# Performance work log

Measured on AMD Instinct MI355X. Metric: run time of the kernel, lower is better.

Reference implementation:

```python
import jax, jax.numpy as jnp
import numpy as np

D = 1024
H = 16
HD = D // H
FF = 4096
B = 4
S = 1024
EPS = 1e-5


def layer_norm(x, g, b):
    mu = jnp.mean(x, axis=-1, keepdims=True)
    var = jnp.mean(jnp.square(x - mu), axis=-1, keepdims=True)
    return (x - mu) * jax.lax.rsqrt(var + EPS) * g + b


def setup_inputs() -> dict:
    key = jax.random.key(0)
    ks = jax.random.split(key, 16)
    s = 0.02
    return {
        "src": jax.random.normal(ks[0], (B, S, D), jnp.float32),
        "attn_bias": jax.random.normal(ks[1], (H, S, S), jnp.float32),
        "Wqkv": jax.random.normal(ks[2], (3 * D, D), jnp.float32) * s,
        "bqkv": jnp.zeros((3 * D,), jnp.float32),
        "Wo": jax.random.normal(ks[3], (D, D), jnp.float32) * s,
        "bo": jnp.zeros((D,), jnp.float32),
        "g1": jnp.ones((D,), jnp.float32),
        "b1n": jnp.zeros((D,), jnp.float32),
        "g2": jnp.ones((D,), jnp.float32),
        "b2n": jnp.zeros((D,), jnp.float32),
        "W1": jax.random.normal(ks[4], (FF, D), jnp.float32) * s,
        "b1": jnp.zeros((FF,), jnp.float32),
        "W2": jax.random.normal(ks[5], (D, FF), jnp.float32) * s,
        "b2": jnp.zeros((D,), jnp.float32),
    }


def reference(src, attn_bias, Wqkv, bqkv, Wo, bo, g1, b1n, g2, b2n, W1, b1, W2, b2):
    bsz, seq, _ = src.shape
    qkv = src @ Wqkv.T + bqkv                      # [B,S,3D]
    q, k, v = jnp.split(qkv, 3, axis=-1)
    q = q.reshape(bsz, seq, H, HD)
    k = k.reshape(bsz, seq, H, HD)
    v = v.reshape(bsz, seq, H, HD)
    scores = jnp.einsum('bthd,bshd->bhts', q, k) / np.sqrt(HD).astype(np.float32)
    scores = scores + attn_bias[None]              # 3D bias broadcast over batch
    w = jax.nn.softmax(scores, axis=-1)
    ctx = jnp.einsum('bhts,bshd->bthd', w, v).reshape(bsz, seq, D)
    attn_out = ctx @ Wo.T + bo
    x = layer_norm(src + attn_out, g1, b1n)
    ff = (jax.nn.gelu(x @ W1.T + b1, approximate=False)) @ W2.T + b2
    return layer_norm(x + ff, g2, b2n)
```

## Files before the change

### kernel.cpp

```cpp
#include <hip/hip_runtime.h>
#include <cstdint>

typedef unsigned short u16;
typedef __bf16 bf16x8 __attribute__((ext_vector_type(8)));
typedef float f32x4 __attribute__((ext_vector_type(4)));
typedef unsigned short u16x8 __attribute__((ext_vector_type(8)));
typedef unsigned short u16x4 __attribute__((ext_vector_type(4)));

__device__ __forceinline__ u16 f2b(float f) {
  union { float f; unsigned u; } x; x.f = f;
  unsigned r = (x.u + 0x7FFFu + ((x.u >> 16) & 1u)) >> 16;
  return (u16)r;
}
__device__ __forceinline__ float b2f(u16 v) {
  union { unsigned u; float f; } x; x.u = (unsigned)v << 16; return x.f;
}

__device__ __forceinline__ void gload_lds16(const void* g, void* l) {
  __builtin_amdgcn_global_load_lds(
      (__attribute__((address_space(1))) void*)(uintptr_t)g,
      (__attribute__((address_space(3))) void*)(uintptr_t)l, 16, 0, 0);
}

struct CastArgs {
  const float* in[5];
  u16* out[5];
  int cum[6];
};
__global__ void cast_multi(CastArgs a) {
  const int i = blockIdx.x * 256 + threadIdx.x;
  int r = 0;
#pragma unroll
  for (int k = 1; k < 5; ++k) r += (i >= a.cum[k]);
  const int local = i - a.cum[r];
  const float4 v = *(const float4*)(a.in[r] + (size_t)local * 4);
  u16x4 o = {f2b(v.x), f2b(v.y), f2b(v.z), f2b(v.w)};
  *(u16x4*)(a.out[r] + (size_t)local * 4) = o;
}

template<bool GELU_ACT, bool WRITE_VT>
__global__ void gemm_nt(const u16* __restrict__ A, const u16* __restrict__ Bw,
                        const float* __restrict__ bias, u16* __restrict__ Cb,
                        u16* __restrict__ Vt, int M, int N, int K) {
  __shared__ u16 As[2][128 * 32];
  __shared__ u16 Bs[2][128 * 32];
  const int tid = threadIdx.x;
  const int lane = tid & 63, wid = tid >> 6;
  const int bm = blockIdx.y * 128, bn = blockIdx.x * 128;
  const int wm = wid >> 1, wn = wid & 1;
  const int r = lane & 15, g = lane >> 4;
  const int s4 = (r >> 1) & 3;

  auto stage = [&](int buf, int k0) {
#pragma unroll
    for (int i = 0; i < 2; ++i) {
      const int c = tid + i * 256;
      const int row = c >> 2, ch = c & 3;
      const int gs = ch ^ ((row >> 1) & 3);
      gload_lds16(A + (size_t)(bm + row) * K + k0 + gs * 8, &As[buf][c * 8]);
      gload_lds16(Bw + (size_t)(bn + row) * K + k0 + gs * 8, &Bs[buf][c * 8]);
    }
  };

  f32x4 acc[4][4] = {};
  stage(0, 0);
  __syncthreads();
  const int nk = K >> 5;
  int cur = 0;
  for (int kt = 0; kt < nk; ++kt) {
    if (kt + 1 < nk) stage(cur ^ 1, (kt + 1) * 32);
    bf16x8 af[4], bfr[4];
#pragma unroll
    for (int m = 0; m < 4; ++m)
      af[m] = *(const bf16x8*)&As[cur][(wm * 64 + m * 16 + r) * 32 + (g ^ s4) * 8];
#pragma unroll
    for (int n = 0; n < 4; ++n)
      bfr[n] = *(const bf16x8*)&Bs[cur][(wn * 64 + n * 16 + r) * 32 + (g ^ s4) * 8];
#pragma unroll
    for (int m = 0; m < 4; ++m)
#pragma unroll
      for (int n = 0; n < 4; ++n)
        acc[m][n] = __builtin_amdgcn_mfma_f32_16x16x32_bf16(af[m], bfr[n], acc[m][n], 0, 0, 0);
    __syncthreads();
    cur ^= 1;
  }
#pragma unroll
  for (int m = 0; m < 4; ++m) {
    const int row0 = bm + wm * 64 + m * 16 + g * 4;
#pragma unroll
    for (int n = 0; n < 4; ++n) {
      const int col = bn + wn * 64 + n * 16 + r;
      const float bv = bias[col];
      if (WRITE_VT && col >= 2048) {
        const int hv = col - 2048;
        const int bb = row0 >> 10, s0 = row0 & 1023;
        u16x4 ov;
#pragma unroll
        for (int j = 0; j < 4; ++j) ov[j] = f2b(acc[m][n][j] + bv);
        *(u16x4*)(Vt + (((size_t)(bb * 16 + (hv >> 6))) * 64 + (hv & 63)) * 1024 + s0) = ov;
      } else {
#pragma unroll
        for (int j = 0; j < 4; ++j) {
          float v = acc[m][n][j] + bv;
          if (GELU_ACT) v = 0.5f * v * (1.f + erff(v * 0.70710678118654752f));
          Cb[(size_t)(row0 + j) * N + col] = f2b(v);
        }
      }
    }
  }
}

__global__ void gemm_nt_splitk(const u16* __restrict__ A, const u16* __restrict__ Bw,
                               float* __restrict__ parts, int M, int N, int K, int Kc) {
  __shared__ u16 As[2][128 * 32];
  __shared__ u16 Bs[2][128 * 32];
  const int tid = threadIdx.x;
  const int lane = tid & 63, wid = tid >> 6;
  const int bm = blockIdx.y * 128, bn = blockIdx.x * 128;
  const int kbase = blockIdx.z * Kc;
  const int wm = wid >> 1, wn = wid & 1;
  const int r = lane & 15, g = lane >> 4;
  const int s4 = (r >> 1) & 3;

  auto stage = [&](int buf, int k0) {
#pragma unroll
    for (int i = 0; i < 2; ++i) {
      const int c = tid + i * 256;
      const int row = c >> 2, ch = c & 3;
      const int gs = ch ^ ((row >> 1) & 3);
      gload_lds16(A + (size_t)(bm + row) * K + k0 + gs * 8, &As[buf][c * 8]);
      gload_lds16(Bw + (size_t)(bn + row) * K + k0 + gs * 8, &Bs[buf][c * 8]);
    }
  };

  f32x4 acc[4][4] = {};
  stage(0, kbase);
  __syncthreads();
  const int nk = Kc >> 5;
  int cur = 0;
  for (int kt = 0; kt < nk; ++kt) {
    if (kt + 1 < nk) stage(cur ^ 1, kbase + (kt + 1) * 32);
    bf16x8 af[4], bfr[4];
#pragma unroll
    for (int m = 0; m < 4; ++m)
      af[m] = *(const bf16x8*)&As[cur][(wm * 64 + m * 16 + r) * 32 + (g ^ s4) * 8];
#pragma unroll
    for (int n = 0; n < 4; ++n)
      bfr[n] = *(const bf16x8*)&Bs[cur][(wn * 64 + n * 16 + r) * 32 + (g ^ s4) * 8];
#pragma unroll
    for (int m = 0; m < 4; ++m)
#pragma unroll
      for (int n = 0; n < 4; ++n)
        acc[m][n] = __builtin_amdgcn_mfma_f32_16x16x32_bf16(af[m], bfr[n], acc[m][n], 0, 0, 0);
    __syncthreads();
    cur ^= 1;
  }
  float* Cp = parts + (size_t)blockIdx.z * M * N;
#pragma unroll
  for (int m = 0; m < 4; ++m) {
    const int row0 = bm + wm * 64 + m * 16 + g * 4;
#pragma unroll
    for (int n = 0; n < 4; ++n) {
      const int col = bn + wn * 64 + n * 16 + r;
#pragma unroll
      for (int j = 0; j < 4; ++j)
        Cp[(size_t)(row0 + j) * N + col] = acc[m][n][j];
    }
  }
}

__global__ __launch_bounds__(256) void attn_kernel(
    const u16* __restrict__ qkv, const u16* __restrict__ Vt,
    const float* __restrict__ bias, u16* __restrict__ ctx) {
  const int fid = blockIdx.x;
  const int xcd = fid & 7, slot = fid >> 3;
  const int G = xcd * 64 + (slot >> 2);
  const int b = slot & 3;
  const int h = G >> 5;
  const int q0 = (G & 31) * 32;
  const int tid = threadIdx.x;
  const int lane = tid & 63, wid = tid >> 6;
  const int r = lane & 15, g = lane >> 4;
  const int bh = b * 16 + h;

  __shared__ __align__(16) u16 PB[2][16 * 1024];

  const size_t qb0 = (size_t)(b * 1024 + q0 + r) * 3072 + h * 64;
  const size_t qb1 = (size_t)(b * 1024 + q0 + 16 + r) * 3072 + h * 64;
  const bf16x8 aq00 = *(const bf16x8*)(qkv + qb0 + g * 8);
  const bf16x8 aq01 = *(const bf16x8*)(qkv + qb0 + 32 + g * 8);
  const bf16x8 aq10 = *(const bf16x8*)(qkv + qb1 + g * 8);
  const bf16x8 aq11 = *(const bf16x8*)(qkv + qb1 + 32 + g * 8);

  const int n0 = wid * 256;

  const u16* kptr = qkv + (size_t)(b * 1024 + n0 + r) * 3072 + 1024 + h * 64;
  const size_t kstep = (size_t)16 * 3072;
  bf16x8 k0a = *(const bf16x8*)(kptr + g * 8);
  bf16x8 k1a = *(const bf16x8*)(kptr + 32 + g * 8);
#pragma unroll
  for (int nt = 0; nt < 16; ++nt) {
    bf16x8 k0b, k1b;
    if (nt + 1 < 16) {
      const u16* kn = kptr + (size_t)(nt + 1) * kstep;
      k0b = *(const bf16x8*)(kn + g * 8);
      k1b = *(const bf16x8*)(kn + 32 + g * 8);
    }
    f32x4 a0 = {0.f, 0.f, 0.f, 0.f}, a1 = {0.f, 0.f, 0.f, 0.f};
    a0 = __builtin_amdgcn_mfma_f32_16x16x32_bf16(k0a, aq00, a0, 0, 0, 0);
    a1 = __builtin_amdgcn_mfma_f32_16x16x32_bf16(k0a, aq10, a1, 0, 0, 0);
    a0 = __builtin_amdgcn_mfma_f32_16x16x32_bf16(k1a, aq01, a0, 0, 0, 0);
    a1 = __builtin_amdgcn_mfma_f32_16x16x32_bf16(k1a, aq11, a1, 0, 0, 0);
    const int col = n0 + nt * 16 + g * 4;
    const int idx = r * 1024 + (col ^ ((r & 15) << 3));
    u16x4 o0 = {f2b(a0[0] * 0.125f), f2b(a0[1] * 0.125f),
                f2b(a0[2] * 0.125f), f2b(a0[3] * 0.125f)};
    u16x4 o1 = {f2b(a1[0] * 0.125f), f2b(a1[1] * 0.125f),
                f2b(a1[2] * 0.125f), f2b(a1[3] * 0.125f)};
    *(u16x4*)&PB[0][idx] = o0;
    *(u16x4*)&PB[1][idx] = o1;
    k0a = k0b;
    k1a = k1b;
  }
  __syncthreads();

#pragma unroll
  for (int tr = 0; tr < 8; ++tr) {
    const int t = tr & 1, rr = tr >> 1;
    const int row = wid * 4 + rr;
    const int swz = (row & 15) << 3;
    u16* prow = &PB[t][row * 1024];
    const float* brow = bias + ((size_t)h * 1024 + q0 + t * 16 + row) * 1024;
    const int c0 = lane * 16;
    float bb[16];
    *(float4*)&bb[0]  = *(const float4*)(brow + c0);
    *(float4*)&bb[4]  = *(const float4*)(brow + c0 + 4);
    *(float4*)&bb[8]  = *(const float4*)(brow + c0 + 8);
    *(float4*)&bb[12] = *(const float4*)(brow + c0 + 12);
    const u16x8 v0 = *(const u16x8*)&prow[c0 ^ swz];
    const u16x8 v1 = *(const u16x8*)&prow[(c0 + 8) ^ swz];
    float f[16];
#pragma unroll
    for (int k = 0; k < 8; ++k) {
      f[k]     = b2f(v0[k]) + bb[k];
      f[8 + k] = b2f(v1[k]) + bb[8 + k];
    }
    float m = f[0];
#pragma unroll
    for (int k = 1; k < 16; ++k) m = fmaxf(m, f[k]);
    m = fmaxf(m, __shfl_xor(m, 1));  m = fmaxf(m, __shfl_xor(m, 2));
    m = fmaxf(m, __shfl_xor(m, 4));  m = fmaxf(m, __shfl_xor(m, 8));
    m = fmaxf(m, __shfl_xor(m, 16)); m = fmaxf(m, __shfl_xor(m, 32));
    float s = 0.f;
#pragma unroll
    for (int k = 0; k < 16; ++k) { f[k] = __expf(f[k] - m); s += f[k]; }
    s += __shfl_xor(s, 1);  s += __shfl_xor(s, 2);
    s += __shfl_xor(s, 4);  s += __shfl_xor(s, 8);
    s += __shfl_xor(s, 16); s += __shfl_xor(s, 32);
    const float inv = 1.f / s;
    u16x8 o0, o1;
#pragma unroll
    for (int k = 0; k < 8; ++k) {
      o0[k] = f2b(f[k] * inv);
      o1[k] = f2b(f[8 + k] * inv);
    }
    *(u16x8*)&prow[c0 ^ swz] = o0;
    *(u16x8*)&prow[(c0 + 8) ^ swz] = o1;
  }
  __syncthreads();

  f32x4 oa = {0.f, 0.f, 0.f, 0.f}, ob = {0.f, 0.f, 0.f, 0.f};
  const u16* vrow = Vt + ((size_t)bh * 64 + wid * 16 + r) * 1024;
  bf16x8 vba = *(const bf16x8*)(vrow + g * 8);
#pragma unroll
  for (int ks = 0; ks < 32; ++ks) {
    bf16x8 vbb;
    if (ks + 1 < 32) vbb = *(const bf16x8*)(vrow + (ks + 1) * 32 + g * 8);
    const int off = (ks * 32 + g * 8) ^ ((r & 15) << 3);
    const bf16x8 pa0 = *(const bf16x8*)&PB[0][r * 1024 + off];
    const bf16x8 pa1 = *(const bf16x8*)&PB[1][r * 1024 + off];
    oa = __builtin_amdgcn_mfma_f32_16x16x32_bf16(pa0, vba, oa, 0, 0, 0);
    ob = __builtin_amdgcn_mfma_f32_16x16x32_bf16(pa1, vba, ob, 0, 0, 0);
    vba = vbb;
  }
#pragma unroll
  for (int j = 0; j < 4; ++j) {
    ctx[(size_t)(b * 1024 + q0 + g * 4 + j) * 1024 + h * 64 + wid * 16 + r] = f2b(oa[j]);
    ctx[(size_t)(b * 1024 + q0 + 16 + g * 4 + j) * 1024 + h * 64 + wid * 16 + r] = f2b(ob[j]);
  }
}

template<int NP, bool RESID_BF16>
__global__ void ln_sum_kernel(const float* __restrict__ parts,
                              const void* __restrict__ resid,
                              const float* __restrict__ cbias,
                              const float* __restrict__ gw, const float* __restrict__ bw,
                              float* __restrict__ outf, u16* __restrict__ outb) {
  const int row = blockIdx.x, tid = threadIdx.x;
  const size_t off = (size_t)row * 1024 + tid * 4;
  float4 v;
  if (RESID_BF16) {
    const u16x4 rb = *(const u16x4*)((const u16*)resid + off);
    v.x = b2f(rb[0]); v.y = b2f(rb[1]); v.z = b2f(rb[2]); v.w = b2f(rb[3]);
  } else {
    v = *(const float4*)((const float*)resid + off);
  }
  const float4 cb = *(const float4*)(cbias + tid * 4);
  v.x += cb.x; v.y += cb.y; v.z += cb.z; v.w += cb.w;
#pragma unroll
  for (int p = 0; p < NP; ++p) {
    const float4 a = *(const float4*)(parts + (size_t)p * 4096 * 1024 + off);
    v.x += a.x; v.y += a.y; v.z += a.z; v.w += a.w;
  }
  float s = v.x + v.y + v.z + v.w;
  float q = v.x * v.x + v.y * v.y + v.z * v.z + v.w * v.w;
#pragma unroll
  for (int m = 32; m >= 1; m >>= 1) { s += __shfl_xor(s, m); q += __shfl_xor(q, m); }
  __shared__ float rs[4], rq[4];
  if ((tid & 63) == 0) { rs[tid >> 6] = s; rq[tid >> 6] = q; }
  __syncthreads();
  s = rs[0] + rs[1] + rs[2] + rs[3];
  q = rq[0] + rq[1] + rq[2] + rq[3];
  const float mu = s * (1.f / 1024.f);
  const float inv = rsqrtf(q * (1.f / 1024.f) - mu * mu + 1e-5f);
  const float4 g4 = *(const float4*)(gw + tid * 4);
  const float4 b4 = *(const float4*)(bw + tid * 4);
  float4 o;
  o.x = (v.x - mu) * inv * g4.x + b4.x;
  o.y = (v.y - mu) * inv * g4.y + b4.y;
  o.z = (v.z - mu) * inv * g4.z + b4.z;
  o.w = (v.w - mu) * inv * g4.w + b4.w;
  if (outf) *(float4*)(outf + off) = o;
  if (outb) {
    u16x4 ob = {f2b(o.x), f2b(o.y), f2b(o.z), f2b(o.w)};
    *(u16x4*)(outb + off) = ob;
  }
}

extern "C" void kernel_launch(void* const* d_in, const int* in_sizes, int n_in,
                              void* d_out, int out_size, void* d_ws, size_t ws_size,
                              hipStream_t stream) {
  (void)in_sizes; (void)n_in; (void)out_size; (void)ws_size;
  const float* src   = (const float*)d_in[0];
  const float* abias = (const float*)d_in[1];
  const float* Wqkv  = (const float*)d_in[2];
  const float* bqkv  = (const float*)d_in[3];
  const float* Wo    = (const float*)d_in[4];
  const float* bo    = (const float*)d_in[5];
  const float* g1    = (const float*)d_in[6];
  const float* b1n   = (const float*)d_in[7];
  const float* g2    = (const float*)d_in[8];
  const float* b2n   = (const float*)d_in[9];
  const float* W1    = (const float*)d_in[10];
  const float* b1    = (const float*)d_in[11];
  const float* W2    = (const float*)d_in[12];
  const float* b2    = (const float*)d_in[13];
  float* out = (float*)d_out;

  char* ws = (char*)d_ws;
  const size_t MB = 1024 * 1024;
  u16* srcb  = (u16*)(ws + 0 * MB);
  u16* ctxb  = (u16*)(ws + 0 * MB);
  u16* xb    = (u16*)(ws + 0 * MB);
  u16* Wqkvb = (u16*)(ws + 8 * MB);
  u16* Wob   = (u16*)(ws + 14 * MB);
  u16* W2b   = (u16*)(ws + 24 * MB);
  u16* qkvb  = (u16*)(ws + 32 * MB);
  u16* Vt    = (u16*)(ws + 56 * MB);
  u16* hb    = (u16*)(ws + 32 * MB);
  float* parts = (float*)(ws + 64 * MB);
  u16* W1b   = (u16*)(ws + 96 * MB);

  CastArgs ca;
  ca.in[0] = src;  ca.out[0] = srcb;
  ca.in[1] = Wqkv; ca.out[1] = Wqkvb;
  ca.in[2] = Wo;   ca.out[2] = Wob;
  ca.in[3] = W1;   ca.out[3] = W1b;
  ca.in[4] = W2;   ca.out[4] = W2b;
  ca.cum[0] = 0;
  ca.cum[1] = 1048576;
  ca.cum[2] = 1048576 + 786432;
  ca.cum[3] = 1048576 + 786432 + 262144;
  ca.cum[4] = 1048576 + 786432 + 262144 + 1048576;
  ca.cum[5] = 4194304;
  cast_multi<<<4194304 / 256, 256, 0, stream>>>(ca);

  gemm_nt<false, true><<<dim3(3072 / 128, 4096 / 128), 256, 0, stream>>>(
      srcb, Wqkvb, bqkv, qkvb, Vt, 4096, 3072, 1024);
  attn_kernel<<<2048, 256, 0, stream>>>(qkvb, Vt, abias, ctxb);
  gemm_nt_splitk<<<dim3(1024 / 128, 4096 / 128, 2), 256, 0, stream>>>(
      ctxb, Wob, parts, 4096, 1024, 1024, 512);
  ln_sum_kernel<2, false><<<4096, 256, 0, stream>>>(
      parts, src, bo, g1, b1n, nullptr, xb);
  gemm_nt<true, false><<<dim3(4096 / 128, 4096 / 128), 256, 0, stream>>>(
      xb, W1b, b1, hb, nullptr, 4096, 4096, 1024);
  gemm_nt_splitk<<<dim3(1024 / 128, 4096 / 128, 2), 256, 0, stream>>>(
      hb, W2b, parts, 4096, 1024, 4096, 2048);
  ln_sum_kernel<2, true><<<4096, 256, 0, stream>>>(
      parts, xb, b2, g2, b2n, out, nullptr);
}
```

Before: 277.8 us.

## Replace 128x128 GEMM with 256x256 eight-wave pipelined tile kernel

The QKV and FF1 GEMMs move to a new kernel: 512 threads, 256x256 output tiles, K-steps of 64, an 8-way XOR-swizzled LDS layout, and global-to-LDS staging split into four chunks interleaved with the MFMA phases. Explicit barriers, waitcnts and setprio around the MFMA blocks are meant to overlap loads with compute and raise operand reuse per LDS byte. The cost is 128KB of LDS per block, so only one block fits per CU. The QKV GEMM also launches just 192 blocks, which may leave some CUs idle.

```diff
diff --git a/kernel.cpp b/kernel.cpp
--- a/kernel.cpp
+++ b/kernel.cpp
@@ -39,54 +39,95 @@
 }
 
 template<bool GELU_ACT, bool WRITE_VT>
-__global__ void gemm_nt(const u16* __restrict__ A, const u16* __restrict__ Bw,
-                        const float* __restrict__ bias, u16* __restrict__ Cb,
-                        u16* __restrict__ Vt, int M, int N, int K) {
-  __shared__ u16 As[2][128 * 32];
-  __shared__ u16 Bs[2][128 * 32];
+__global__ __launch_bounds__(512, 2) void gemm_nt_256(
+    const u16* __restrict__ A, const u16* __restrict__ Bw,
+    const float* __restrict__ bias, u16* __restrict__ Cb,
+    u16* __restrict__ Vt, int M, int N, int K) {
+  __shared__ u16 As[2][256 * 64];
+  __shared__ u16 Bs[2][256 * 64];
   const int tid = threadIdx.x;
   const int lane = tid & 63, wid = tid >> 6;
-  const int bm = blockIdx.y * 128, bn = blockIdx.x * 128;
-  const int wm = wid >> 1, wn = wid & 1;
+  const int bm = blockIdx.y * 256, bn = blockIdx.x * 256;
+  const int wm = wid >> 2, wn = wid & 3;
   const int r = lane & 15, g = lane >> 4;
-  const int s4 = (r >> 1) & 3;
-
-  auto stage = [&](int buf, int k0) {
+
+  auto stage_unit = [&](int buf, int kt, int which) {
+    const int k0 = kt * 64;
 #pragma unroll
     for (int i = 0; i < 2; ++i) {
-      const int c = tid + i * 256;
-      const int row = c >> 2, ch = c & 3;
-      const int gs = ch ^ ((row >> 1) & 3);
-      gload_lds16(A + (size_t)(bm + row) * K + k0 + gs * 8, &As[buf][c * 8]);
-      gload_lds16(Bw + (size_t)(bn + row) * K + k0 + gs * 8, &Bs[buf][c * 8]);
+      const int j = (wid * 2 + i) * 64 + lane;
+      const int rowu = j >> 3, c = j & 7;
+      const int gs = c ^ (rowu & 7);
+      if (which < 2) {
+        const int row = which * 128 + rowu;
+        gload_lds16(A + (size_t)(bm + row) * K + k0 + gs * 8,
+                    &As[buf][row * 64 + c * 8]);
+      } else {
+        const int row = (which - 2) * 128 + rowu;
+        gload_lds16(Bw + (size_t)(bn + row) * K + k0 + gs * 8,
+                    &Bs[buf][row * 64 + c * 8]);
+      }
     }
   };
 
-  f32x4 acc[4][4] = {};
-  stage(0, 0);
-  __syncthreads();
-  const int nk = K >> 5;
-  int cur = 0;
-  for (int kt = 0; kt < nk; ++kt) {
-    if (kt + 1 < nk) stage(cur ^ 1, (kt + 1) * 32);
-    bf16x8 af[4], bfr[4];
-#pragma unroll
-    for (int m = 0; m < 4; ++m)
-      af[m] = *(const bf16x8*)&As[cur][(wm * 64 + m * 16 + r) * 32 + (g ^ s4) * 8];
-#pragma unroll
-    for (int n = 0; n < 4; ++n)
-      bfr[n] = *(const bf16x8*)&Bs[cur][(wn * 64 + n * 16 + r) * 32 + (g ^ s4) * 8];
-#pragma unroll
-    for (int m = 0; m < 4; ++m)
-#pragma unroll
-      for (int n = 0; n < 4; ++n)
-        acc[m][n] = __builtin_amdgcn_mfma_f32_16x16x32_bf16(af[m], bfr[n], acc[m][n], 0, 0, 0);
-    __syncthreads();
-    cur ^= 1;
-  }
-#pragma unroll
-  for (int m = 0; m < 4; ++m) {
-    const int row0 = bm + wm * 64 + m * 16 + g * 4;
+  f32x4 acc[8][4] = {};
+  stage_unit(0, 0, 0); stage_unit(0, 0, 1); stage_unit(0, 0, 2); stage_unit(0, 0, 3);
+  stage_unit(1, 1, 2); stage_unit(1, 1, 3);
+  asm volatile("s_waitcnt vmcnt(4)" ::: "memory");
+  __builtin_amdgcn_s_barrier();
+  __builtin_amdgcn_sched_barrier(0);
+
+  const int nkt = K >> 6;
+  bf16x8 bfr[2][4];
+  for (int kt = 0; kt < nkt; ++kt) {
+    const int buf = kt & 1;
+    const u16* as = &As[buf][0];
+    const u16* bs = &Bs[buf][0];
+#pragma unroll
+    for (int q = 0; q < 4; ++q) {
+      const int mh = q >> 1, ks = q & 1;
+      bf16x8 af[4];
+#pragma unroll
+      for (int m2 = 0; m2 < 4; ++m2) {
+        const int row = wm * 128 + mh * 64 + m2 * 16 + r;
+        af[m2] = *(const bf16x8*)&as[row * 64 + ((ks * 4 + g) ^ (row & 7)) * 8];
+      }
+      if (mh == 0) {
+#pragma unroll
+        for (int n = 0; n < 4; ++n) {
+          const int row = wn * 64 + n * 16 + r;
+          bfr[ks][n] = *(const bf16x8*)&bs[row * 64 + ((ks * 4 + g) ^ (row & 7)) * 8];
+        }
+      }
+      if (q == 0)      { if (kt + 1 < nkt) stage_unit(buf ^ 1, kt + 1, 0); }
+      else if (q == 1) { if (kt + 1 < nkt) stage_unit(buf ^ 1, kt + 1, 1); }
+      else if (q == 2) { if (kt + 2 < nkt) stage_unit(buf,     kt + 2, 2); }
+      else             { if (kt + 2 < nkt) stage_unit(buf,     kt + 2, 3); }
+
+      __builtin_amdgcn_s_barrier();
+      asm volatile("s_waitcnt lgkmcnt(0)" ::: "memory");
+      __builtin_amdgcn_sched_barrier(0);
+      __builtin_amdgcn_s_setprio(1);
+#pragma unroll
+      for (int m2 = 0; m2 < 4; ++m2)
+#pragma unroll
+        for (int n = 0; n < 4; ++n)
+          acc[mh * 4 + m2][n] = __builtin_amdgcn_mfma_f32_16x16x32_bf16(
+              af[m2], bfr[ks][n], acc[mh * 4 + m2][n], 0, 0, 0);
+      __builtin_amdgcn_s_setprio(0);
+      __builtin_amdgcn_sched_barrier(0);
+      if (q == 3) {
+        if (kt + 2 < nkt)      asm volatile("s_waitcnt vmcnt(4)" ::: "memory");
+        else if (kt + 1 < nkt) asm volatile("s_waitcnt vmcnt(0)" ::: "memory");
+      }
+      __builtin_amdgcn_s_barrier();
+      __builtin_amdgcn_sched_barrier(0);
+    }
+  }
+
+#pragma unroll
+  for (int m = 0; m < 8; ++m) {
+    const int row0 = bm + wm * 128 + m * 16 + g * 4;
 #pragma unroll
     for (int n = 0; n < 4; ++n) {
       const int col = bn + wn * 64 + n * 16 + r;
@@ -385,14 +426,14 @@
   ca.cum[5] = 4194304;
   cast_multi<<<4194304 / 256, 256, 0, stream>>>(ca);
 
-  gemm_nt<false, true><<<dim3(3072 / 128, 4096 / 128), 256, 0, stream>>>(
+  gemm_nt_256<false, true><<<dim3(3072 / 256, 4096 / 256), 512, 0, stream>>>(
       srcb, Wqkvb, bqkv, qkvb, Vt, 4096, 3072, 1024);
   attn_kernel<<<2048, 256, 0, stream>>>(qkvb, Vt, abias, ctxb);
   gemm_nt_splitk<<<dim3(1024 / 128, 4096 / 128, 2), 256, 0, stream>>>(
       ctxb, Wob, parts, 4096, 1024, 1024, 512);
   ln_sum_kernel<2, false><<<4096, 256, 0, stream>>>(
       parts, src, bo, g1, b1n, nullptr, xb);
-  gemm_nt<true, false><<<dim3(4096 / 128, 4096 / 128), 256, 0, stream>>>(
+  gemm_nt_256<true, false><<<dim3(4096 / 256, 4096 / 256), 512, 0, stream>>>(
       xb, W1b, b1, hb, nullptr, 4096, 4096, 1024);
   gemm_nt_splitk<<<dim3(1024 / 128, 4096 / 128, 2), 256, 0, stream>>>(
       hb, W2b, parts, 4096, 1024, 4096, 2048);
```

Measured after the change: 327.2 us. 1.18x slower.
